# Performance work log

Hardware: AMD Instinct MI355X
Metric: run time of the kernel (lower is better)

## Reference

```python
import jax, jax.numpy as jnp
import numpy as np

B = 8192
NUM_DRUGS = 4000
NUM_CELL_LINES = 64
D0 = 128
D1 = 128


def setup_inputs() -> dict:
    key = jax.random.key(0)
    k1, k2, k3, k4, k5 = jax.random.split(key, 5)
    drug_pairs = jax.random.randint(k1, (B, 2), 0, NUM_DRUGS, dtype=jnp.int64)
    cell_lines = jax.random.randint(k2, (B,), 0, NUM_CELL_LINES, dtype=jnp.int64)
    h_drug = jax.random.normal(k3, (NUM_DRUGS, D0), dtype=jnp.float32)
    predictor_lin = 0.01 * jax.random.normal(k4, (NUM_CELL_LINES, D0, D1), dtype=jnp.float32)
    predictor_prod = 0.01 * jax.random.normal(k5, (NUM_CELL_LINES, D1, D1), dtype=jnp.float32)
    return {"drug_pairs": drug_pairs, "cell_lines": cell_lines, "h_drug": h_drug,
            "predictor_lin": predictor_lin, "predictor_prod": predictor_prod}


def reference(drug_pairs, cell_lines, h_drug, predictor_lin, predictor_prod):
    # Gather per-sample cell-line-specific linear weights: [B, D0, D1]
    W = predictor_lin[cell_lines]
    h1 = h_drug[drug_pairs[:, 0]]  # [B, D0]
    h2 = h_drug[drug_pairs[:, 1]]  # [B, D0]
    h1 = jax.nn.relu(jnp.einsum('bd,bdh->bh', h1, W))  # [B, D1]
    h2 = jax.nn.relu(jnp.einsum('bd,bdh->bh', h2, W))  # [B, D1]
    # Symmetric bilinear form G = P + P^T, per sample
    P = predictor_prod[cell_lines]  # [B, D1, D1]
    G = P + jnp.swapaxes(P, 1, 2)
    # score = <h1, G h2>
    return jnp.einsum('bh,bhk,bk->b', h1, G, h2)
```

## Files before the change

kernel.cpp:

```cpp
#include <hip/hip_runtime.h>

#define D        128
#define CH       4
#define TPB      512
#define LIST_CAP 256

__global__ __launch_bounds__(TPB, 1) void ipp_main(
    const int* __restrict__ dp, const int* __restrict__ cl,
    const float* __restrict__ hd, const float* __restrict__ W_all,
    const float* __restrict__ P_all, float* __restrict__ out,
    int B, int range, int ch)
{
    extern __shared__ float smem[];
    float4* sW4    = (float4*)smem;
    float4* sP4    = sW4 + 4096;
    float*  sx1    = smem + 32768;
    float*  sx2    = sx1 + 256;
    float*  sh1    = sx2 + 256;
    float*  sh2    = sh1 + 256;
    float4* part1  = (float4*)(sh2 + 256);
    float4* part2  = part1 + 256;
    int*    list   = (int*)(part2 + 256);
    int*    lcount = list + LIST_CAP;
    float*  sred   = (float*)(lcount + 1);

    const int tid   = threadIdx.x;
    const int c     = blockIdx.x / ch;
    const int chunk = blockIdx.x % ch;
    const int sub   = tid >> 8;
    const int stid  = tid & 255;
    const int g     = stid >> 5;
    const int c4    = stid & 31;
    const int wsub  = stid >> 6;

    if (tid == 0) *lcount = 0;
    __syncthreads();

    {
        const int base = chunk * range;
        const int end  = min(base + range, B);
        for (int j = base + tid; j < end; j += TPB)
            if (cl[j] == c) {
                int p = atomicAdd(lcount, 1);
                if (p < LIST_CAP) list[p] = j;
            }
    }
    {
        const float4* gW = (const float4*)(W_all + (size_t)c * D * D);
        const float4* gP = (const float4*)(P_all + (size_t)c * D * D);
        for (int i = tid; i < 4096; i += TPB) sW4[i] = gW[i];
        for (int i = tid; i < 4096; i += TPB) sP4[i] = gP[i];
    }
    __syncthreads();
    const int n = min(*lcount, LIST_CAP);

#define MATVEC_DUAL(SRCA, SRCB, MAT, OUTA, OUTB)                               \
    {                                                                          \
        float4 a1 = {0,0,0,0}, a2 = {0,0,0,0};                                 \
        const float4* xa = (const float4*)(SRCA);                              \
        const float4* xb = (const float4*)(SRCB);                              \
        const int q0 = g * 4;                                                  \
        _Pragma("unroll")                                                      \
        for (int q = 0; q < 4; ++q) {                                          \
            const float4 v1 = xa[q0 + q];                                      \
            const float4 v2 = xb[q0 + q];                                      \
            const int db = (q0 + q) * 4;                                       \
            const float4 w0 = (MAT)[(db+0)*32 + c4];                           \
            const float4 w1 = (MAT)[(db+1)*32 + c4];                           \
            const float4 w2 = (MAT)[(db+2)*32 + c4];                           \
            const float4 w3 = (MAT)[(db+3)*32 + c4];                           \
            a1.x = fmaf(v1.x, w0.x, a1.x); a2.x = fmaf(v2.x, w0.x, a2.x);      \
            a1.y = fmaf(v1.x, w0.y, a1.y); a2.y = fmaf(v2.x, w0.y, a2.y);      \
            a1.z = fmaf(v1.x, w0.z, a1.z); a2.z = fmaf(v2.x, w0.z, a2.z);      \
            a1.w = fmaf(v1.x, w0.w, a1.w); a2.w = fmaf(v2.x, w0.w, a2.w);      \
            a1.x = fmaf(v1.y, w1.x, a1.x); a2.x = fmaf(v2.y, w1.x, a2.x);      \
            a1.y = fmaf(v1.y, w1.y, a1.y); a2.y = fmaf(v2.y, w1.y, a2.y);      \
            a1.z = fmaf(v1.y, w1.z, a1.z); a2.z = fmaf(v2.y, w1.z, a2.z);      \
            a1.w = fmaf(v1.y, w1.w, a1.w); a2.w = fmaf(v2.y, w1.w, a2.w);      \
            a1.x = fmaf(v1.z, w2.x, a1.x); a2.x = fmaf(v2.z, w2.x, a2.x);      \
            a1.y = fmaf(v1.z, w2.y, a1.y); a2.y = fmaf(v2.z, w2.y, a2.y);      \
            a1.z = fmaf(v1.z, w2.z, a1.z); a2.z = fmaf(v2.z, w2.z, a2.z);      \
            a1.w = fmaf(v1.z, w2.w, a1.w); a2.w = fmaf(v2.z, w2.w, a2.w);      \
            a1.x = fmaf(v1.w, w3.x, a1.x); a2.x = fmaf(v2.w, w3.x, a2.x);      \
            a1.y = fmaf(v1.w, w3.y, a1.y); a2.y = fmaf(v2.w, w3.y, a2.y);      \
            a1.z = fmaf(v1.w, w3.z, a1.z); a2.z = fmaf(v2.w, w3.z, a2.z);      \
            a1.w = fmaf(v1.w, w3.w, a1.w); a2.w = fmaf(v2.w, w3.w, a2.w);      \
        }                                                                      \
        a1.x += __shfl_xor(a1.x, 32, 64); a2.x += __shfl_xor(a2.x, 32, 64);    \
        a1.y += __shfl_xor(a1.y, 32, 64); a2.y += __shfl_xor(a2.y, 32, 64);    \
        a1.z += __shfl_xor(a1.z, 32, 64); a2.z += __shfl_xor(a2.z, 32, 64);    \
        a1.w += __shfl_xor(a1.w, 32, 64); a2.w += __shfl_xor(a2.w, 32, 64);    \
        if ((tid & 32) == 0) {                                                 \
            (OUTA)[sub*128 + wsub*32 + c4] = a1;                               \
            (OUTB)[sub*128 + wsub*32 + c4] = a2;                               \
        }                                                                      \
    }

    const int iters = (n + 1) >> 1;
    for (int it = 0; it < iters; ++it) {
        const int  p      = it * 2 + sub;
        const bool active = p < n;
        const int  b      = list[active ? p : 0];

        if (stid < D) sx1[sub*D + stid]       = hd[(size_t)dp[2*b]   * D + stid];
        else          sx2[sub*D + (stid - D)] = hd[(size_t)dp[2*b+1] * D + (stid - D)];
        __syncthreads();

        MATVEC_DUAL(sx1 + sub*D, sx2 + sub*D, sW4, part1, part2)
        __syncthreads();
        {
            const int k = stid & 127;
            const float* pp = (const float*)((stid < D) ? part1 : part2) + sub*512;
            float s = 0.f;
            #pragma unroll
            for (int w = 0; w < 4; ++w) s += pp[w*128 + k];
            s = fmaxf(s, 0.f);
            if (stid < D) sh1[sub*D + k] = s; else sh2[sub*D + k] = s;
        }
        __syncthreads();

        MATVEC_DUAL(sh1 + sub*D, sh2 + sub*D, sP4, part1, part2)
        __syncthreads();

        float partial;
        {
            const int k = stid & 127;
            const float* pp = (const float*)((stid < D) ? part1 : part2) + sub*512;
            const float* hv = (stid < D) ? (sh2 + sub*D) : (sh1 + sub*D);
            float s = 0.f;
            #pragma unroll
            for (int w = 0; w < 4; ++w) s += pp[w*128 + k];
            partial = s * hv[k];
        }
        #pragma unroll
        for (int off = 32; off; off >>= 1)
            partial += __shfl_down(partial, off, 64);
        if ((tid & 63) == 0) sred[sub*4 + wsub] = partial;
        __syncthreads();
        if (stid == 0 && active)
            out[b] = sred[sub*4] + sred[sub*4+1] + sred[sub*4+2] + sred[sub*4+3];
    }
#undef MATVEC_DUAL
}

extern "C" void kernel_launch(void* const* d_in, const int* in_sizes, int n_in,
                              void* d_out, int out_size, void* d_ws, size_t ws_size,
                              hipStream_t stream) {
    const int*   dp    = (const int*)  d_in[0];
    const int*   cl    = (const int*)  d_in[1];
    const float* hd    = (const float*)d_in[2];
    const float* W_all = (const float*)d_in[3];
    const float* P_all = (const float*)d_in[4];
    float*       out   = (float*)d_out;

    const int B     = out_size;
    const int ncl   = in_sizes[4] / (D * D);
    const int range = (B + CH - 1) / CH;

    constexpr size_t SMEM = 144448;
    (void)hipFuncSetAttribute((const void*)ipp_main,
                              hipFuncAttributeMaxDynamicSharedMemorySize,
                              (int)SMEM);
    ipp_main<<<dim3(ncl * CH), dim3(TPB), SMEM, stream>>>(
        dp, cl, hd, W_all, P_all, out, B, range, CH);
}
```

Baseline: 129.9 us.

## Keep per-cell-line W and P tiles in registers and batch four samples per pass

Each thread now loads its 16-row slice of the W and P matrices into registers once, replacing the 128 KB shared-memory copies. Each pass processes four samples (eight vectors) against those register tiles. The grid doubles to 8 chunks per cell line with 256-thread blocks, two blocks per CU. This cuts shared-memory weight traffic and raises block count and occupancy, at the cost of heavy register pressure (128 floats of weights plus accumulators), which may cause spills. LIST_CAP is lowered to 128 per chunk; that holds for the test distribution of about 16 samples per chunk but would silently drop samples under skewed inputs.

Result: faster. 112.1 us (-13.7%).

```diff
diff --git a/kernel.cpp b/kernel.cpp
--- a/kernel.cpp
+++ b/kernel.cpp
@@ -1,39 +1,31 @@
 #include <hip/hip_runtime.h>
 
 #define D        128
-#define CH       4
-#define TPB      512
-#define LIST_CAP 256
+#define CH       8
+#define TPB      256
+#define EPP      4
+#define LIST_CAP 128
 
-__global__ __launch_bounds__(TPB, 1) void ipp_main(
+__global__ __launch_bounds__(TPB, 2) void ipp_main(
     const int* __restrict__ dp, const int* __restrict__ cl,
     const float* __restrict__ hd, const float* __restrict__ W_all,
     const float* __restrict__ P_all, float* __restrict__ out,
-    int B, int range, int ch)
+    int B, int range)
 {
-    extern __shared__ float smem[];
-    float4* sW4    = (float4*)smem;
-    float4* sP4    = sW4 + 4096;
-    float*  sx1    = smem + 32768;
-    float*  sx2    = sx1 + 256;
-    float*  sh1    = sx2 + 256;
-    float*  sh2    = sh1 + 256;
-    float4* part1  = (float4*)(sh2 + 256);
-    float4* part2  = part1 + 256;
-    int*    list   = (int*)(part2 + 256);
-    int*    lcount = list + LIST_CAP;
-    float*  sred   = (float*)(lcount + 1);
+    __shared__ float  sx[8][D];
+    __shared__ float  sh[8][D];
+    __shared__ float4 part[4][8][32];
+    __shared__ int    list[LIST_CAP];
+    __shared__ int    lcount;
 
     const int tid   = threadIdx.x;
-    const int c     = blockIdx.x / ch;
-    const int chunk = blockIdx.x % ch;
-    const int sub   = tid >> 8;
-    const int stid  = tid & 255;
-    const int g     = stid >> 5;
-    const int c4    = stid & 31;
-    const int wsub  = stid >> 6;
+    const int c     = blockIdx.x / CH;
+    const int chunk = blockIdx.x % CH;
+    const int g     = tid >> 5;
+    const int c4    = tid & 31;
+    const int wv    = tid >> 6;
 
-    if (tid == 0) *lcount = 0;
+    if (tid == 0) lcount = 0;
     __syncthreads();
 
     {
@@ -41,106 +33,131 @@
         const int end  = min(base + range, B);
         for (int j = base + tid; j < end; j += TPB)
             if (cl[j] == c) {
-                int p = atomicAdd(lcount, 1);
+                int p = atomicAdd(&lcount, 1);
                 if (p < LIST_CAP) list[p] = j;
             }
     }
+
+    float4 Wreg[16], Preg[16];
     {
         const float4* gW = (const float4*)(W_all + (size_t)c * D * D);
         const float4* gP = (const float4*)(P_all + (size_t)c * D * D);
-        for (int i = tid; i < 4096; i += TPB) sW4[i] = gW[i];
-        for (int i = tid; i < 4096; i += TPB) sP4[i] = gP[i];
+        #pragma unroll
+        for (int dd = 0; dd < 16; ++dd) {
+            Wreg[dd] = gW[(g * 16 + dd) * 32 + c4];
+            Preg[dd] = gP[(g * 16 + dd) * 32 + c4];
+        }
     }
     __syncthreads();
-    const int n = min(*lcount, LIST_CAP);
+    const int n = min(lcount, LIST_CAP);
 
-#define MATVEC_DUAL(SRCA, SRCB, MAT, OUTA, OUTB)                               \
+#define FMA4(A_, S_, W_)                                                       \
+    (A_).x = fmaf((S_), (W_).x, (A_).x);                                       \
+    (A_).y = fmaf((S_), (W_).y, (A_).y);                                       \
+    (A_).z = fmaf((S_), (W_).z, (A_).z);                                       \
+    (A_).w = fmaf((S_), (W_).w, (A_).w);
+
+#define MATTILE(SRC, REG)                                                      \
     {                                                                          \
-        float4 a1 = {0,0,0,0}, a2 = {0,0,0,0};                                 \
-        const float4* xa = (const float4*)(SRCA);                              \
-        const float4* xb = (const float4*)(SRCB);                              \
-        const int q0 = g * 4;                                                  \
         _Pragma("unroll")                                                      \
         for (int q = 0; q < 4; ++q) {                                          \
-            const float4 v1 = xa[q0 + q];                                      \
-            const float4 v2 = xb[q0 + q];                                      \
-            const int db = (q0 + q) * 4;                                       \
-            const float4 w0 = (MAT)[(db+0)*32 + c4];                           \
-            const float4 w1 = (MAT)[(db+1)*32 + c4];                           \
-            const float4 w2 = (MAT)[(db+2)*32 + c4];                           \
-            const float4 w3 = (MAT)[(db+3)*32 + c4];                           \
-            a1.x = fmaf(v1.x, w0.x, a1.x); a2.x = fmaf(v2.x, w0.x, a2.x);      \
-            a1.y = fmaf(v1.x, w0.y, a1.y); a2.y = fmaf(v2.x, w0.y, a2.y);      \
-            a1.z = fmaf(v1.x, w0.z, a1.z); a2.z = fmaf(v2.x, w0.z, a2.z);      \
-            a1.w = fmaf(v1.x, w0.w, a1.w); a2.w = fmaf(v2.x, w0.w, a2.w);      \
-            a1.x = fmaf(v1.y, w1.x, a1.x); a2.x = fmaf(v2.y, w1.x, a2.x);      \
-            a1.y = fmaf(v1.y, w1.y, a1.y); a2.y = fmaf(v2.y, w1.y, a2.y);      \
-            a1.z = fmaf(v1.y, w1.z, a1.z); a2.z = fmaf(v2.y, w1.z, a2.z);      \
-            a1.w = fmaf(v1.y, w1.w, a1.w); a2.w = fmaf(v2.y, w1.w, a2.w);      \
-            a1.x = fmaf(v1.z, w2.x, a1.x); a2.x = fmaf(v2.z, w2.x, a2.x);      \
-            a1.y = fmaf(v1.z, w2.y, a1.y); a2.y = fmaf(v2.z, w2.y, a2.y);      \
-            a1.z = fmaf(v1.z, w2.z, a1.z); a2.z = fmaf(v2.z, w2.z, a2.z);      \
-            a1.w = fmaf(v1.z, w2.w, a1.w); a2.w = fmaf(v2.z, w2.w, a2.w);      \
-            a1.x = fmaf(v1.w, w3.x, a1.x); a2.x = fmaf(v2.w, w3.x, a2.x);      \
-            a1.y = fmaf(v1.w, w3.y, a1.y); a2.y = fmaf(v2.w, w3.y, a2.y);      \
-            a1.z = fmaf(v1.w, w3.z, a1.z); a2.z = fmaf(v2.w, w3.z, a2.z);      \
-            a1.w = fmaf(v1.w, w3.w, a1.w); a2.w = fmaf(v2.w, w3.w, a2.w);      \
+            _Pragma("unroll")                                                  \
+            for (int r = 0; r < 8; ++r) {                                      \
+                const float4 xq = ((const float4*)(SRC)[r])[g * 4 + q];        \
+                float4& ac = acc[r >> 1][r & 1];                               \
+                FMA4(ac, xq.x, REG[q * 4 + 0])                                 \
+                FMA4(ac, xq.y, REG[q * 4 + 1])                                 \
+                FMA4(ac, xq.z, REG[q * 4 + 2])                                 \
+                FMA4(ac, xq.w, REG[q * 4 + 3])                                 \
+            }                                                                  \
         }                                                                      \
-        a1.x += __shfl_xor(a1.x, 32, 64); a2.x += __shfl_xor(a2.x, 32, 64);    \
-        a1.y += __shfl_xor(a1.y, 32, 64); a2.y += __shfl_xor(a2.y, 32, 64);    \
-        a1.z += __shfl_xor(a1.z, 32, 64); a2.z += __shfl_xor(a2.z, 32, 64);    \
-        a1.w += __shfl_xor(a1.w, 32, 64); a2.w += __shfl_xor(a2.w, 32, 64);    \
+        _Pragma("unroll")                                                      \
+        for (int e = 0; e < EPP; ++e) {                                        \
+            _Pragma("unroll")                                                  \
+            for (int op = 0; op < 2; ++op) {                                   \
+                float4& ac = acc[e][op];                                       \
+                ac.x += __shfl_xor(ac.x, 32, 64);                              \
+                ac.y += __shfl_xor(ac.y, 32, 64);                              \
+                ac.z += __shfl_xor(ac.z, 32, 64);                              \
+                ac.w += __shfl_xor(ac.w, 32, 64);                              \
+            }                                                                  \
+        }                                                                      \
         if ((tid & 32) == 0) {                                                 \
-            (OUTA)[sub*128 + wsub*32 + c4] = a1;                               \
-            (OUTB)[sub*128 + wsub*32 + c4] = a2;                               \
+            _Pragma("unroll")                                                  \
+            for (int r = 0; r < 8; ++r)                                        \
+                part[wv][r][c4] = acc[r >> 1][r & 1];                          \
         }                                                                      \
     }
 
-    const int iters = (n + 1) >> 1;
-    for (int it = 0; it < iters; ++it) {
-        const int  p      = it * 2 + sub;
-        const bool active = p < n;
-        const int  b      = list[active ? p : 0];
+    const int npass = (n + EPP - 1) / EPP;
+    for (int pass = 0; pass < npass; ++pass) {
+        const int pbase = pass * EPP;
 
-        if (stid < D) sx1[sub*D + stid]       = hd[(size_t)dp[2*b]   * D + stid];
-        else          sx2[sub*D + (stid - D)] = hd[(size_t)dp[2*b+1] * D + (stid - D)];
-        __syncthreads();
-
-        MATVEC_DUAL(sx1 + sub*D, sx2 + sub*D, sW4, part1, part2)
-        __syncthreads();
         {
-            const int k = stid & 127;
-            const float* pp = (const float*)((stid < D) ? part1 : part2) + sub*512;
-            float s = 0.f;
-            #pragma unroll
-            for (int w = 0; w < 4; ++w) s += pp[w*128 + k];
-            s = fmaxf(s, 0.f);
-            if (stid < D) sh1[sub*D + k] = s; else sh2[sub*D + k] = s;
+            const int e  = g >> 1, op = g & 1;
+            const int pe = pbase + e;
+            const int b  = list[pe < n ? pe : 0];
+            const int dr = dp[2 * b + op];
+            ((float4*)sx[g])[c4] = ((const float4*)(hd + (size_t)dr * D))[c4];
         }
         __syncthreads();
 
-        MATVEC_DUAL(sh1 + sub*D, sh2 + sub*D, sP4, part1, part2)
+        float4 acc[EPP][2];
+        #pragma unroll
+        for (int e = 0; e < EPP; ++e)
+            #pragma unroll
+            for (int op = 0; op < 2; ++op)
+                acc[e][op] = make_float4(0.f, 0.f, 0.f, 0.f);
+        MATTILE(sx, Wreg)
+        __syncthreads();
+        {
+            const float4 s0 = part[0][g][c4], s1 = part[1][g][c4];
+            const float4 s2 = part[2][g][c4], s3 = part[3][g][c4];
+            float4 s;
+            s.x = fmaxf(s0.x + s1.x + s2.x + s3.x, 0.f);
+            s.y = fmaxf(s0.y + s1.y + s2.y + s3.y, 0.f);
+            s.z = fmaxf(s0.z + s1.z + s2.z + s3.z, 0.f);
+            s.w = fmaxf(s0.w + s1.w + s2.w + s3.w, 0.f);
+            ((float4*)sh[g])[c4] = s;
+        }
         __syncthreads();
 
-        float partial;
+        #pragma unroll
+        for (int e = 0; e < EPP; ++e)
+            #pragma unroll
+            for (int op = 0; op < 2; ++op)
+                acc[e][op] = make_float4(0.f, 0.f, 0.f, 0.f);
+        MATTILE(sh, Preg)
+        __syncthreads();
         {
-            const int k = stid & 127;
-            const float* pp = (const float*)((stid < D) ? part1 : part2) + sub*512;
-            const float* hv = (stid < D) ? (sh2 + sub*D) : (sh1 + sub*D);
-            float s = 0.f;
+            const float4 s0 = part[0][g][c4], s1 = part[1][g][c4];
+            const float4 s2 = part[2][g][c4], s3 = part[3][g][c4];
+            float4 s;
+            s.x = s0.x + s1.x + s2.x + s3.x;
+            s.y = s0.y + s1.y + s2.y + s3.y;
+            s.z = s0.z + s1.z + s2.z + s3.z;
+            s.w = s0.w + s1.w + s2.w + s3.w;
+            ((float4*)sx[g])[c4] = s;
+        }
+        __syncthreads();
+
+        {
+            const int e  = tid >> 6;
+            const int k2 = (tid & 63) * 2;
+            const float* t1 = sx[2 * e],     * t2 = sx[2 * e + 1];
+            const float* h1 = sh[2 * e],     * h2 = sh[2 * e + 1];
+            float prt = t1[k2] * h2[k2] + t1[k2 + 1] * h2[k2 + 1]
+                      + t2[k2] * h1[k2] + t2[k2 + 1] * h1[k2 + 1];
             #pragma unroll
-            for (int w = 0; w < 4; ++w) s += pp[w*128 + k];
-            partial = s * hv[k];
+            for (int off = 32; off; off >>= 1)
+                prt += __shfl_down(prt, off, 64);
+            const int pe = pbase + e;
+            if ((tid & 63) == 0 && pe < n) out[list[pe]] = prt;
         }
-        #pragma unroll
-        for (int off = 32; off; off >>= 1)
-            partial += __shfl_down(partial, off, 64);
-        if ((tid & 63) == 0) sred[sub*4 + wsub] = partial;
         __syncthreads();
-        if (stid == 0 && active)
-            out[b] = sred[sub*4] + sred[sub*4+1] + sred[sub*4+2] + sred[sub*4+3];
     }
-#undef MATVEC_DUAL
+#undef MATTILE
+#undef FMA4
 }
 
 extern "C" void kernel_launch(void* const* d_in, const int* in_sizes, int n_in,
@@ -157,10 +174,6 @@
     const int ncl   = in_sizes[4] / (D * D);
     const int range = (B + CH - 1) / CH;
 
-    constexpr size_t SMEM = 144448;
-    (void)hipFuncSetAttribute((const void*)ipp_main,
-                              hipFuncAttributeMaxDynamicSharedMemorySize,
-                              (int)SMEM);
-    ipp_main<<<dim3(ncl * CH), dim3(TPB), SMEM, stream>>>(
-        dp, cl, hd, W_all, P_all, out, B, range, CH);
+    ipp_main<<<dim3(ncl * CH), dim3(TPB), 0, stream>>>(
+        dp, cl, hd, W_all, P_all, out, B, range);
 }
```
